# Optimization experiments

Hardware: AMD Instinct MI355X
Metric: run time of the kernel (lower is better)

## Reference

```python
import jax, jax.numpy as jnp
import numpy as np

N_NODES = 50000
N_EDGES = 800000
IN_DIM = 128
HID = 8
HEADS = 8
OUT_DIM = 64
NEG_SLOPE = 0.2


def setup_inputs() -> dict:
    key = jax.random.key(0)
    ks = jax.random.split(key, 8)
    x = jax.random.normal(ks[0], (N_NODES, IN_DIM), dtype=jnp.float32)
    edge_index = jax.random.randint(ks[1], (2, N_EDGES), 0, N_NODES, dtype=jnp.int64)
    W1 = jax.random.normal(ks[2], (IN_DIM, HEADS * HID), dtype=jnp.float32) / np.sqrt(IN_DIM)
    a_src1 = jax.random.normal(ks[3], (HEADS, HID), dtype=jnp.float32)
    a_dst1 = jax.random.normal(ks[4], (HEADS, HID), dtype=jnp.float32)
    b1 = jnp.zeros((HEADS * HID,), dtype=jnp.float32)
    W2 = jax.random.normal(ks[5], (HEADS * HID, OUT_DIM), dtype=jnp.float32) / np.sqrt(HEADS * HID)
    a_src2 = jax.random.normal(ks[6], (1, OUT_DIM), dtype=jnp.float32)
    a_dst2 = jax.random.normal(ks[7], (1, OUT_DIM), dtype=jnp.float32)
    b2 = jnp.zeros((OUT_DIM,), dtype=jnp.float32)
    return {"x": x, "edge_index": edge_index, "W1": W1, "a_src1": a_src1,
            "a_dst1": a_dst1, "b1": b1, "W2": W2, "a_src2": a_src2,
            "a_dst2": a_dst2, "b2": b2}


def gat_conv(x, src, dst, W, a_src, a_dst, b, heads, ch):
    # PyG GATConv (eval mode): linear -> per-edge LeakyReLU score ->
    # segment-softmax over incoming edges -> weighted scatter-add -> +bias
    n = x.shape[0]
    h = (x @ W).reshape(n, heads, ch)               # [N,H,C]
    score_src = jnp.einsum('nhc,hc->nh', h, a_src)  # [N,H]
    score_dst = jnp.einsum('nhc,hc->nh', h, a_dst)  # [N,H]
    e = jax.nn.leaky_relu(score_src[src] + score_dst[dst], NEG_SLOPE)  # [E,H]
    m = jax.ops.segment_max(e, dst, num_segments=n)
    m = jnp.where(jnp.isfinite(m), m, 0.0)
    p = jnp.exp(e - m[dst])
    denom = jax.ops.segment_sum(p, dst, num_segments=n)
    alpha = p / (denom[dst] + 1e-16)                # [E,H]
    out = jax.ops.segment_sum(h[src] * alpha[:, :, None], dst, num_segments=n)
    return out.reshape(n, heads * ch) + b


def reference(x, edge_index, W1, a_src1, a_dst1, b1, W2, a_src2, a_dst2, b2):
    n = x.shape[0]
    # add_self_loops=True (PyG default)
    loops = jnp.arange(n, dtype=edge_index.dtype)
    src = jnp.concatenate([edge_index[0], loops])
    dst = jnp.concatenate([edge_index[1], loops])
    h = gat_conv(x, src, dst, W1, a_src1, a_dst1, b1, HEADS, HID)
    h = jax.nn.elu(h)
    out = gat_conv(h, src, dst, W2, a_src2, a_dst2, b2, 1, OUT_DIM)
    return out
```

## Files before the change

### kernel.cpp

```cpp
#include <hip/hip_runtime.h>
#include <hip/hip_fp16.h>
#include <math.h>

#define N_NODES 50000
#define N_EDGES 800000
#define ET (N_EDGES + N_NODES)
#define IN_DIM 128
#define H1DIM 64
#define HEADS 8
#define HID 8
#define OUT_DIM 64
#define NEG_SLOPE 0.2f

#define SCAN_TILE 256
#define NTILES ((N_NODES + SCAN_TILE - 1) / SCAN_TILE)
#define RC 8
#define PF 6

#define LIN1_WAVES (N_NODES / 8)
#define LIN1_BLOCKS ((LIN1_WAVES + 3) / 4)
#define EB ((ET + 255) / 256)

__device__ __forceinline__ float lrelu(float v) { return v >= 0.f ? v : NEG_SLOPE * v; }

__device__ __forceinline__ float rdlane(float v, int l) {
    return __int_as_float(__builtin_amdgcn_readlane(__float_as_int(v), l));
}

__device__ __forceinline__ void fma8raw(uint4 u, float alpha, float* a) {
    float2 f0 = __half22float2(*(const __half2*)&u.x);
    float2 f1 = __half22float2(*(const __half2*)&u.y);
    float2 f2 = __half22float2(*(const __half2*)&u.z);
    float2 f3 = __half22float2(*(const __half2*)&u.w);
    a[0] += f0.x * alpha; a[1] += f0.y * alpha;
    a[2] += f1.x * alpha; a[3] += f1.y * alpha;
    a[4] += f2.x * alpha; a[5] += f2.y * alpha;
    a[6] += f3.x * alpha; a[7] += f3.y * alpha;
}

__device__ __forceinline__ void fma8h(const __half* __restrict__ base, float alpha, float* a) {
    fma8raw(*reinterpret_cast<const uint4*>(base), alpha, a);
}

__device__ __forceinline__ void edge_nodes(const int* __restrict__ ei, int e, int& s, int& d) {
    if (e < N_EDGES) { s = ei[e]; d = ei[N_EDGES + e]; }
    else             { s = e - N_EDGES; d = s; }
}


__global__ __launch_bounds__(256) void cl1_kernel(
    const int* __restrict__ ei, int* __restrict__ cnt, int* __restrict__ pos,
    const float* __restrict__ x, const float* __restrict__ W1,
    const float* __restrict__ a_src, const float* __restrict__ a_dst,
    __half* __restrict__ h1, float* __restrict__ ssrc, float* __restrict__ sdst)
{
    if (blockIdx.x >= LIN1_BLOCKS) {
        int i = (blockIdx.x - LIN1_BLOCKS) * 256 + threadIdx.x;
        if (i >= ET) return;
        int s, d; edge_nodes(ei, i, s, d);
        pos[i] = atomicAdd(&cnt[d], 1);
        return;
    }
    int wid = threadIdx.x >> 6, t = threadIdx.x & 63;
    int g = blockIdx.x * 4 + wid;
    if (g >= LIN1_WAVES) return;
    int n0 = g * 8;

    float x0[8], x1[8];
    #pragma unroll
    for (int nn = 0; nn < 8; ++nn) {
        x0[nn] = x[(n0 + nn) * IN_DIM + t];
        x1[nn] = x[(n0 + nn) * IN_DIM + 64 + t];
    }
    float acc[8] = {0,0,0,0,0,0,0,0};
    #pragma unroll 8
    for (int k = 0; k < 64; ++k) {
        float w = W1[k * 64 + t];
        #pragma unroll
        for (int nn = 0; nn < 8; ++nn) acc[nn] += rdlane(x0[nn], k) * w;
    }
    #pragma unroll 8
    for (int k = 0; k < 64; ++k) {
        float w = W1[(k + 64) * 64 + t];
        #pragma unroll
        for (int nn = 0; nn < 8; ++nn) acc[nn] += rdlane(x1[nn], k) * w;
    }

    float av = a_src[t], bv = a_dst[t];
    #pragma unroll
    for (int nn = 0; nn < 8; ++nn) {
        int n = n0 + nn;
        h1[n * 64 + t] = __float2half(acc[nn]);
        float rs = acc[nn] * av, rd = acc[nn] * bv;
        rs += __shfl_xor(rs, 1); rs += __shfl_xor(rs, 2); rs += __shfl_xor(rs, 4);
        rd += __shfl_xor(rd, 1); rd += __shfl_xor(rd, 2); rd += __shfl_xor(rd, 4);
        if ((t & 7) == 0) { ssrc[n * 8 + (t >> 3)] = rs; sdst[n * 8 + (t >> 3)] = rd; }
    }
}


__global__ __launch_bounds__(SCAN_TILE) void scanA_kernel(
    const int* __restrict__ cnt, int* __restrict__ row, int* __restrict__ aux)
{
    __shared__ int sh[SCAN_TILE];
    int t = threadIdx.x, i = blockIdx.x * SCAN_TILE + t;
    int v = (i < N_NODES) ? cnt[i] : 0;
    sh[t] = v;
    __syncthreads();
    #pragma unroll
    for (int off = 1; off < SCAN_TILE; off <<= 1) {
        int add = (t >= off) ? sh[t - off] : 0;
        __syncthreads();
        sh[t] += add;
        __syncthreads();
    }
    if (i < N_NODES) row[i] = sh[t] - v;
    if (t == SCAN_TILE - 1) aux[blockIdx.x] = sh[t];
}

__global__ __launch_bounds__(SCAN_TILE) void scanB_kernel(int* __restrict__ aux, int* __restrict__ row) {
    __shared__ int sh[SCAN_TILE];
    int t = threadIdx.x;
    int v = (t < NTILES) ? aux[t] : 0;
    sh[t] = v;
    __syncthreads();
    #pragma unroll
    for (int off = 1; off < SCAN_TILE; off <<= 1) {
        int add = (t >= off) ? sh[t - off] : 0;
        __syncthreads();
        sh[t] += add;
        __syncthreads();
    }
    if (t < NTILES) aux[t] = sh[t] - v;
    if (t == NTILES - 1) row[N_NODES] = sh[t];
}

__global__ __launch_bounds__(SCAN_TILE) void scanC_kernel(
    const int* __restrict__ aux, int* __restrict__ row)
{
    int i = blockIdx.x * SCAN_TILE + threadIdx.x;
    if (i >= N_NODES) return;
    row[i] += aux[i >> 8];
}

__global__ void fill_kernel(const int* __restrict__ ei, const int* __restrict__ row,
                            const int* __restrict__ pos, int* __restrict__ adj)
{
    int i = blockIdx.x * blockDim.x + threadIdx.x;
    if (i >= ET) return;
    int s, d; edge_nodes(ei, i, s, d);
    adj[row[d] + pos[i]] = s;
}


__global__ __launch_bounds__(256) void l1_kernel(
    const int* __restrict__ row, const int* __restrict__ adj,
    const __half* __restrict__ h1, const float* __restrict__ s1, const float* __restrict__ t1,
    const float* __restrict__ b1, const float* __restrict__ W2,
    const float* __restrict__ as2, const float* __restrict__ ad2,
    __half* __restrict__ h2, float* __restrict__ s2, float* __restrict__ t2)
{
    int wid = threadIdx.x >> 6, t = threadIdx.x & 63;
    int half = t >> 5, tt = t & 31;
    int n = blockIdx.x * 8 + wid * 2 + half;
    int beg = row[n], end = row[n + 1];
    int slot = tt >> 3, h = tt & 7;
    float sd = t1[n * 8 + h];
    const int e0 = beg + slot;
    const int hb = half << 5;

    int   sv[RC];
    float p[RC];
    uint4 raw[PF];
    float m = -3e38f;
    #pragma unroll
    for (int it = 0; it < RC; ++it) {
        int e = e0 + it * 4;
        bool ok = e < end;
        int s = ok ? adj[e] : n;
        sv[it] = s;
        float v = ok ? lrelu(s1[s * 8 + h] + sd) : -3e38f;
        p[it] = v;
        m = fmaxf(m, v);
        if (it < PF) raw[it] = *reinterpret_cast<const uint4*>(h1 + (size_t)s * 64 + h * 8);
    }
    for (int e = e0 + RC * 4; e < end; e += 4)
        m = fmaxf(m, lrelu(s1[adj[e] * 8 + h] + sd));
    m = fmaxf(m, __shfl_xor(m, 8));
    m = fmaxf(m, __shfl_xor(m, 16));

    float den = 0.f;
    #pragma unroll
    for (int it = 0; it < RC; ++it) {
        float pe = __expf(p[it] - m);
        p[it] = pe;
        den += pe;
    }
    for (int e = e0 + RC * 4; e < end; e += 4)
        den += __expf(lrelu(s1[adj[e] * 8 + h] + sd) - m);
    den += __shfl_xor(den, 8);
    den += __shfl_xor(den, 16);
    float inv = 1.f / (den + 1e-16f);

    float a[8] = {0,0,0,0,0,0,0,0};
    #pragma unroll
    for (int it = 0; it < PF; ++it) fma8raw(raw[it], p[it] * inv, a);
    #pragma unroll
    for (int it = PF; it < RC; ++it) {
        int e = e0 + it * 4;
        if (e < end) fma8h(h1 + (size_t)sv[it] * 64 + h * 8, p[it] * inv, a);
    }
    for (int e = e0 + RC * 4; e < end; e += 4) {
        int s = adj[e];
        float alpha = __expf(lrelu(s1[s * 8 + h] + sd) - m) * inv;
        fma8h(h1 + (size_t)s * 64 + h * 8, alpha, a);
    }
    #pragma unroll
    for (int j = 0; j < 8; ++j) {
        a[j] += __shfl_xor(a[j], 8);
        a[j] += __shfl_xor(a[j], 16);
    }

    float ha0 = 0.f, ha1 = 0.f;
    int srcA = hb + (tt >> 3);
    #pragma unroll
    for (int j = 0; j < 8; ++j) {
        float vA = __shfl(a[j], srcA);
        float vB = __shfl(a[j], srcA + 4);
        if ((tt & 7) == j) { ha0 = vA; ha1 = vB; }
    }

    ha0 += b1[tt];
    ha1 += b1[tt + 32];
    ha0 = ha0 > 0.f ? ha0 : (__expf(ha0) - 1.f);
    ha1 = ha1 > 0.f ? ha1 : (__expf(ha1) - 1.f);

    float c0 = 0.f, c1 = 0.f;
    #pragma unroll 8
    for (int k = 0; k < 32; ++k) {
        float w = __shfl(ha0, hb + k);
        c0 += w * W2[k * 64 + tt];
        c1 += w * W2[k * 64 + tt + 32];
    }
    #pragma unroll 8
    for (int k = 0; k < 32; ++k) {
        float w = __shfl(ha1, hb + k);
        c0 += w * W2[(k + 32) * 64 + tt];
        c1 += w * W2[(k + 32) * 64 + tt + 32];
    }
    h2[n * 64 + tt]      = __float2half(c0);
    h2[n * 64 + tt + 32] = __float2half(c1);

    float rs = c0 * as2[tt] + c1 * as2[tt + 32];
    float rd = c0 * ad2[tt] + c1 * ad2[tt + 32];
    #pragma unroll
    for (int mk = 16; mk >= 1; mk >>= 1) {
        rs += __shfl_xor(rs, mk);
        rd += __shfl_xor(rd, mk);
    }
    if (tt == 0) { s2[n] = rs; t2[n] = rd; }
}


__global__ __launch_bounds__(256) void l2_kernel(
    const int* __restrict__ row, const int* __restrict__ adj,
    const __half* __restrict__ h2, const float* __restrict__ s2, const float* __restrict__ t2,
    const float* __restrict__ b2, float* __restrict__ out)
{
    int wid = threadIdx.x >> 6, t = threadIdx.x & 63;
    int half = t >> 5, tt = t & 31;
    int n = blockIdx.x * 8 + wid * 2 + half;
    int beg = row[n], end = row[n + 1];
    int slot = tt >> 3, g = tt & 7;
    float sd = t2[n];
    const int e0 = beg + slot;

    int   sv[RC];
    float p[RC];
    uint4 raw[PF];
    float m = -3e38f;
    #pragma unroll
    for (int it = 0; it < RC; ++it) {
        int e = e0 + it * 4;
        bool ok = e < end;
        int s = ok ? adj[e] : n;
        sv[it] = s;
        float v = ok ? lrelu(s2[s] + sd) : -3e38f;
        p[it] = v;
        m = fmaxf(m, v);
        if (it < PF) raw[it] = *reinterpret_cast<const uint4*>(h2 + (size_t)s * 64 + g * 8);
    }
    for (int e = e0 + RC * 4; e < end; e += 4)
        m = fmaxf(m, lrelu(s2[adj[e]] + sd));
    m = fmaxf(m, __shfl_xor(m, 8));
    m = fmaxf(m, __shfl_xor(m, 16));

    float den = 0.f;
    #pragma unroll
    for (int it = 0; it < RC; ++it) {
        float pe = __expf(p[it] - m);
        p[it] = pe;
        den += pe;
    }
    for (int e = e0 + RC * 4; e < end; e += 4)
        den += __expf(lrelu(s2[adj[e]] + sd) - m);
    den += __shfl_xor(den, 8);
    den += __shfl_xor(den, 16);
    float inv = 1.f / (den + 1e-16f);

    float a[8] = {0,0,0,0,0,0,0,0};
    #pragma unroll
    for (int it = 0; it < PF; ++it) fma8raw(raw[it], p[it] * inv, a);
    #pragma unroll
    for (int it = PF; it < RC; ++it) {
        int e = e0 + it * 4;
        if (e < end) fma8h(h2 + (size_t)sv[it] * 64 + g * 8, p[it] * inv, a);
    }
    for (int e = e0 + RC * 4; e < end; e += 4) {
        int s = adj[e];
        float alpha = __expf(lrelu(s2[s] + sd) - m) * inv;
        fma8h(h2 + (size_t)s * 64 + g * 8, alpha, a);
    }
    #pragma unroll
    for (int j = 0; j < 8; ++j) {
        a[j] += __shfl_xor(a[j], 8);
        a[j] += __shfl_xor(a[j], 16);
    }
    if (slot == 0) {
        float4 o0 = make_float4(a[0] + b2[g * 8 + 0], a[1] + b2[g * 8 + 1],
                                a[2] + b2[g * 8 + 2], a[3] + b2[g * 8 + 3]);
        float4 o1 = make_float4(a[4] + b2[g * 8 + 4], a[5] + b2[g * 8 + 5],
                                a[6] + b2[g * 8 + 6], a[7] + b2[g * 8 + 7]);
        float4* op = (float4*)(out + (size_t)n * 64 + g * 8);
        op[0] = o0; op[1] = o1;
    }
}

extern "C" void kernel_launch(void* const* d_in, const int* in_sizes, int n_in,
                              void* d_out, int out_size, void* d_ws, size_t ws_size,
                              hipStream_t stream)
{
    const float* x   = (const float*)d_in[0];
    const int* ei    = (const int*)d_in[1];
    const float* W1  = (const float*)d_in[2];
    const float* as1 = (const float*)d_in[3];
    const float* ad1 = (const float*)d_in[4];
    const float* b1  = (const float*)d_in[5];
    const float* W2  = (const float*)d_in[6];
    const float* as2 = (const float*)d_in[7];
    const float* ad2 = (const float*)d_in[8];
    const float* b2  = (const float*)d_in[9];
    float* out = (float*)d_out;

    char* wsb = (char*)d_ws;
    __half* h1  = (__half*)wsb;
    __half* h2  = h1 + (size_t)N_NODES * 64;
    float*  s1  = (float*)(h2 + (size_t)N_NODES * 64);
    float*  t1  = s1 + N_NODES * 8;
    float*  s2  = t1 + N_NODES * 8;
    float*  t2  = s2 + N_NODES;
    int*    cnt = (int*)(t2 + N_NODES);
    int*    rowp = cnt + N_NODES;
    int*    aux  = rowp + N_NODES + 1;
    int*    adj  = aux + NTILES;
    int*    pos  = adj + ET;

    hipMemsetAsync(cnt, 0, N_NODES * sizeof(int), stream);

    cl1_kernel<<<LIN1_BLOCKS + EB, 256, 0, stream>>>(ei, cnt, pos, x, W1, as1, ad1, h1, s1, t1);

    scanA_kernel<<<NTILES, SCAN_TILE, 0, stream>>>(cnt, rowp, aux);
    scanB_kernel<<<1, SCAN_TILE, 0, stream>>>(aux, rowp);
    scanC_kernel<<<NTILES, SCAN_TILE, 0, stream>>>(aux, rowp);
    fill_kernel<<<EB, 256, 0, stream>>>(ei, rowp, pos, adj);

    l1_kernel<<<N_NODES / 8, 256, 0, stream>>>(rowp, adj, h1, s1, t1,
                                               b1, W2, as2, ad2, h2, s2, t2);

    l2_kernel<<<N_NODES / 8, 256, 0, stream>>>(rowp, adj, h2, s2, t2, b2, out);
}
```

Before: 231.0 us.

## Split degree counters into 8 replicas to spread atomic contention in CSR build

The degree-count atomics now go to one of 8 replicated counter arrays, chosen by block index, instead of a single array. The scan sums the 8 replicas, and scanC computes a per-replica starting offset so fill can place each edge without conflicts. Edge-count blocks are also moved ahead of the linear-layer blocks in the combined launch. This is meant to reduce atomic serialization on hot destination nodes, at the cost of a larger memset and 8x more counter reads and writes in the scans.

```diff
diff --git a/kernel.cpp b/kernel.cpp
--- a/kernel.cpp
+++ b/kernel.cpp
@@ -49,20 +49,20 @@
 
 
 __global__ __launch_bounds__(256) void cl1_kernel(
-    const int* __restrict__ ei, int* __restrict__ cnt, int* __restrict__ pos,
+    const int* __restrict__ ei, int* __restrict__ cnt8, int* __restrict__ pos,
     const float* __restrict__ x, const float* __restrict__ W1,
     const float* __restrict__ a_src, const float* __restrict__ a_dst,
     __half* __restrict__ h1, float* __restrict__ ssrc, float* __restrict__ sdst)
 {
-    if (blockIdx.x >= LIN1_BLOCKS) {
-        int i = (blockIdx.x - LIN1_BLOCKS) * 256 + threadIdx.x;
+    if (blockIdx.x < EB) {
+        int i = blockIdx.x * 256 + threadIdx.x;
         if (i >= ET) return;
         int s, d; edge_nodes(ei, i, s, d);
-        pos[i] = atomicAdd(&cnt[d], 1);
+        pos[i] = atomicAdd(&cnt8[(blockIdx.x & 7) * N_NODES + d], 1);
         return;
     }
     int wid = threadIdx.x >> 6, t = threadIdx.x & 63;
-    int g = blockIdx.x * 4 + wid;
+    int g = (blockIdx.x - EB) * 4 + wid;
     if (g >= LIN1_WAVES) return;
     int n0 = g * 8;
 
@@ -100,11 +100,15 @@
 
 
 __global__ __launch_bounds__(SCAN_TILE) void scanA_kernel(
-    const int* __restrict__ cnt, int* __restrict__ row, int* __restrict__ aux)
+    const int* __restrict__ cnt8, int* __restrict__ row, int* __restrict__ aux)
 {
     __shared__ int sh[SCAN_TILE];
     int t = threadIdx.x, i = blockIdx.x * SCAN_TILE + t;
-    int v = (i < N_NODES) ? cnt[i] : 0;
+    int v = 0;
+    if (i < N_NODES) {
+        #pragma unroll
+        for (int c = 0; c < 8; ++c) v += cnt8[c * N_NODES + i];
+    }
     sh[t] = v;
     __syncthreads();
     #pragma unroll
@@ -136,20 +140,29 @@
 }
 
 __global__ __launch_bounds__(SCAN_TILE) void scanC_kernel(
-    const int* __restrict__ aux, int* __restrict__ row)
+    const int* __restrict__ aux, int* __restrict__ row,
+    const int* __restrict__ cnt8, int* __restrict__ off8)
 {
     int i = blockIdx.x * SCAN_TILE + threadIdx.x;
     if (i >= N_NODES) return;
-    row[i] += aux[i >> 8];
-}
-
-__global__ void fill_kernel(const int* __restrict__ ei, const int* __restrict__ row,
+    int r = row[i] + aux[i >> 8];
+    row[i] = r;
+    int run = r;
+    #pragma unroll
+    for (int c = 0; c < 8; ++c) {
+        off8[c * N_NODES + i] = run;
+        run += cnt8[c * N_NODES + i];
+    }
+}
+
+__global__ void fill_kernel(const int* __restrict__ ei, const int* __restrict__ off8,
                             const int* __restrict__ pos, int* __restrict__ adj)
 {
     int i = blockIdx.x * blockDim.x + threadIdx.x;
     if (i >= ET) return;
     int s, d; edge_nodes(ei, i, s, d);
-    adj[row[d] + pos[i]] = s;
+    int c = (i >> 8) & 7;
+    adj[off8[c * N_NODES + d] + pos[i]] = s;
 }
 
 
@@ -359,20 +372,21 @@
     float*  t1  = s1 + N_NODES * 8;
     float*  s2  = t1 + N_NODES * 8;
     float*  t2  = s2 + N_NODES;
-    int*    cnt = (int*)(t2 + N_NODES);
-    int*    rowp = cnt + N_NODES;
+    int*    cnt8 = (int*)(t2 + N_NODES);
+    int*    off8 = cnt8 + 8 * N_NODES;
+    int*    rowp = off8 + 8 * N_NODES;
     int*    aux  = rowp + N_NODES + 1;
     int*    adj  = aux + NTILES;
     int*    pos  = adj + ET;
 
-    hipMemsetAsync(cnt, 0, N_NODES * sizeof(int), stream);
-
-    cl1_kernel<<<LIN1_BLOCKS + EB, 256, 0, stream>>>(ei, cnt, pos, x, W1, as1, ad1, h1, s1, t1);
-
-    scanA_kernel<<<NTILES, SCAN_TILE, 0, stream>>>(cnt, rowp, aux);
+    hipMemsetAsync(cnt8, 0, 8 * N_NODES * sizeof(int), stream);
+
+    cl1_kernel<<<EB + LIN1_BLOCKS, 256, 0, stream>>>(ei, cnt8, pos, x, W1, as1, ad1, h1, s1, t1);
+
+    scanA_kernel<<<NTILES, SCAN_TILE, 0, stream>>>(cnt8, rowp, aux);
     scanB_kernel<<<1, SCAN_TILE, 0, stream>>>(aux, rowp);
-    scanC_kernel<<<NTILES, SCAN_TILE, 0, stream>>>(aux, rowp);
-    fill_kernel<<<EB, 256, 0, stream>>>(ei, rowp, pos, adj);
+    scanC_kernel<<<NTILES, SCAN_TILE, 0, stream>>>(aux, rowp, cnt8, off8);
+    fill_kernel<<<EB, 256, 0, stream>>>(ei, off8, pos, adj);
 
     l1_kernel<<<N_NODES / 8, 256, 0, stream>>>(rowp, adj, h1, s1, t1,
                                                b1, W2, as2, ad2, h2, s2, t2);
```

After: 248.9 us. 7.7% more time.

## Assign 16 lanes per node in GAT aggregation kernels, four nodes per wave

Applied to the files above, without the earlier changes.

The layer-1 and layer-2 aggregation kernels now map each destination node to 16 lanes (two edge slots times eight head or feature groups) instead of 32. Each wave handles four nodes and the grid is halved. The register-cached edge window grows from 8 to 13 per slot. The early h-row prefetch (PF) is removed, so feature rows are loaded in the accumulation loop. The aim is to cut idle lanes, since average in-degree is about 17, and to halve the cross-lane reduction work. In exchange each lane walks more edges serially, which adds latency per node, and the W2 projection does twice the FMAs per lane.

```diff
diff --git a/kernel.cpp b/kernel.cpp
--- a/kernel.cpp
+++ b/kernel.cpp
@@ -6,16 +6,12 @@
 #define N_EDGES 800000
 #define ET (N_EDGES + N_NODES)
 #define IN_DIM 128
-#define H1DIM 64
 #define HEADS 8
-#define HID 8
-#define OUT_DIM 64
 #define NEG_SLOPE 0.2f
 
 #define SCAN_TILE 256
 #define NTILES ((N_NODES + SCAN_TILE - 1) / SCAN_TILE)
-#define RC 8
-#define PF 6
+#define RC 13
 
 #define LIN1_WAVES (N_NODES / 8)
 #define LIN1_BLOCKS ((LIN1_WAVES + 3) / 4)
@@ -27,7 +23,8 @@
     return __int_as_float(__builtin_amdgcn_readlane(__float_as_int(v), l));
 }
 
-__device__ __forceinline__ void fma8raw(uint4 u, float alpha, float* a) {
+__device__ __forceinline__ void fma8h(const __half* __restrict__ base, float alpha, float* a) {
+    uint4 u = *reinterpret_cast<const uint4*>(base);
     float2 f0 = __half22float2(*(const __half2*)&u.x);
     float2 f1 = __half22float2(*(const __half2*)&u.y);
     float2 f2 = __half22float2(*(const __half2*)&u.z);
@@ -38,10 +35,6 @@
     a[6] += f3.x * alpha; a[7] += f3.y * alpha;
 }
 
-__device__ __forceinline__ void fma8h(const __half* __restrict__ base, float alpha, float* a) {
-    fma8raw(*reinterpret_cast<const uint4*>(base), alpha, a);
-}
-
 __device__ __forceinline__ void edge_nodes(const int* __restrict__ ei, int e, int& s, int& d) {
     if (e < N_EDGES) { s = ei[e]; d = ei[N_EDGES + e]; }
     else             { s = e - N_EDGES; d = s; }
@@ -161,33 +154,30 @@
     __half* __restrict__ h2, float* __restrict__ s2, float* __restrict__ t2)
 {
     int wid = threadIdx.x >> 6, t = threadIdx.x & 63;
-    int half = t >> 5, tt = t & 31;
-    int n = blockIdx.x * 8 + wid * 2 + half;
+    int q = t >> 4, tt = t & 15;
+    int n = blockIdx.x * 16 + wid * 4 + q;
     int beg = row[n], end = row[n + 1];
     int slot = tt >> 3, h = tt & 7;
     float sd = t1[n * 8 + h];
     const int e0 = beg + slot;
-    const int hb = half << 5;
+    const int qb = q << 4;
 
     int   sv[RC];
     float p[RC];
-    uint4 raw[PF];
     float m = -3e38f;
     #pragma unroll
     for (int it = 0; it < RC; ++it) {
-        int e = e0 + it * 4;
+        int e = e0 + it * 2;
         bool ok = e < end;
         int s = ok ? adj[e] : n;
         sv[it] = s;
         float v = ok ? lrelu(s1[s * 8 + h] + sd) : -3e38f;
         p[it] = v;
         m = fmaxf(m, v);
-        if (it < PF) raw[it] = *reinterpret_cast<const uint4*>(h1 + (size_t)s * 64 + h * 8);
-    }
-    for (int e = e0 + RC * 4; e < end; e += 4)
+    }
+    for (int e = e0 + RC * 2; e < end; e += 2)
         m = fmaxf(m, lrelu(s1[adj[e] * 8 + h] + sd));
     m = fmaxf(m, __shfl_xor(m, 8));
-    m = fmaxf(m, __shfl_xor(m, 16));
 
     float den = 0.f;
     #pragma unroll
@@ -196,65 +186,66 @@
         p[it] = pe;
         den += pe;
     }
-    for (int e = e0 + RC * 4; e < end; e += 4)
+    for (int e = e0 + RC * 2; e < end; e += 2)
         den += __expf(lrelu(s1[adj[e] * 8 + h] + sd) - m);
     den += __shfl_xor(den, 8);
-    den += __shfl_xor(den, 16);
     float inv = 1.f / (den + 1e-16f);
 
     float a[8] = {0,0,0,0,0,0,0,0};
     #pragma unroll
-    for (int it = 0; it < PF; ++it) fma8raw(raw[it], p[it] * inv, a);
-    #pragma unroll
-    for (int it = PF; it < RC; ++it) {
-        int e = e0 + it * 4;
+    for (int it = 0; it < RC; ++it) {
+        int e = e0 + it * 2;
         if (e < end) fma8h(h1 + (size_t)sv[it] * 64 + h * 8, p[it] * inv, a);
     }
-    for (int e = e0 + RC * 4; e < end; e += 4) {
+    for (int e = e0 + RC * 2; e < end; e += 2) {
         int s = adj[e];
         float alpha = __expf(lrelu(s1[s * 8 + h] + sd) - m) * inv;
         fma8h(h1 + (size_t)s * 64 + h * 8, alpha, a);
     }
     #pragma unroll
+    for (int j = 0; j < 8; ++j) a[j] += __shfl_xor(a[j], 8);
+
+    float ha[4] = {0,0,0,0};
+    int src0 = qb + (tt >> 3);
+    #pragma unroll
     for (int j = 0; j < 8; ++j) {
-        a[j] += __shfl_xor(a[j], 8);
-        a[j] += __shfl_xor(a[j], 16);
-    }
-
-    float ha0 = 0.f, ha1 = 0.f;
-    int srcA = hb + (tt >> 3);
-    #pragma unroll
-    for (int j = 0; j < 8; ++j) {
-        float vA = __shfl(a[j], srcA);
-        float vB = __shfl(a[j], srcA + 4);
-        if ((tt & 7) == j) { ha0 = vA; ha1 = vB; }
-    }
-
-    ha0 += b1[tt];
-    ha1 += b1[tt + 32];
-    ha0 = ha0 > 0.f ? ha0 : (__expf(ha0) - 1.f);
-    ha1 = ha1 > 0.f ? ha1 : (__expf(ha1) - 1.f);
-
-    float c0 = 0.f, c1 = 0.f;
-    #pragma unroll 8
-    for (int k = 0; k < 32; ++k) {
-        float w = __shfl(ha0, hb + k);
-        c0 += w * W2[k * 64 + tt];
-        c1 += w * W2[k * 64 + tt + 32];
-    }
-    #pragma unroll 8
-    for (int k = 0; k < 32; ++k) {
-        float w = __shfl(ha1, hb + k);
-        c0 += w * W2[(k + 32) * 64 + tt];
-        c1 += w * W2[(k + 32) * 64 + tt + 32];
-    }
-    h2[n * 64 + tt]      = __float2half(c0);
-    h2[n * 64 + tt + 32] = __float2half(c1);
-
-    float rs = c0 * as2[tt] + c1 * as2[tt + 32];
-    float rd = c0 * ad2[tt] + c1 * ad2[tt + 32];
-    #pragma unroll
-    for (int mk = 16; mk >= 1; mk >>= 1) {
+        float v0 = __shfl(a[j], src0);
+        float v1 = __shfl(a[j], src0 + 2);
+        float v2 = __shfl(a[j], src0 + 4);
+        float v3 = __shfl(a[j], src0 + 6);
+        if ((tt & 7) == j) { ha[0] = v0; ha[1] = v1; ha[2] = v2; ha[3] = v3; }
+    }
+
+    #pragma unroll
+    for (int c = 0; c < 4; ++c) {
+        float v = ha[c] + b1[tt + 16 * c];
+        ha[c] = v > 0.f ? v : (__expf(v) - 1.f);
+    }
+
+    float c2[4] = {0,0,0,0};
+    #pragma unroll
+    for (int cr = 0; cr < 4; ++cr) {
+        #pragma unroll 8
+        for (int kk = 0; kk < 16; ++kk) {
+            float w = __shfl(ha[cr], qb + kk);
+            int k = cr * 16 + kk;
+            c2[0] += w * W2[k * 64 + tt];
+            c2[1] += w * W2[k * 64 + tt + 16];
+            c2[2] += w * W2[k * 64 + tt + 32];
+            c2[3] += w * W2[k * 64 + tt + 48];
+        }
+    }
+    #pragma unroll
+    for (int c = 0; c < 4; ++c) h2[n * 64 + tt + 16 * c] = __float2half(c2[c]);
+
+    float rs = 0.f, rd = 0.f;
+    #pragma unroll
+    for (int c = 0; c < 4; ++c) {
+        rs += c2[c] * as2[tt + 16 * c];
+        rd += c2[c] * ad2[tt + 16 * c];
+    }
+    #pragma unroll
+    for (int mk = 8; mk >= 1; mk >>= 1) {
         rs += __shfl_xor(rs, mk);
         rd += __shfl_xor(rd, mk);
     }
@@ -268,8 +259,8 @@
     const float* __restrict__ b2, float* __restrict__ out)
 {
     int wid = threadIdx.x >> 6, t = threadIdx.x & 63;
-    int half = t >> 5, tt = t & 31;
-    int n = blockIdx.x * 8 + wid * 2 + half;
+    int q = t >> 4, tt = t & 15;
+    int n = blockIdx.x * 16 + wid * 4 + q;
     int beg = row[n], end = row[n + 1];
     int slot = tt >> 3, g = tt & 7;
     float sd = t2[n];
@@ -277,23 +268,20 @@
 
     int   sv[RC];
     float p[RC];
-    uint4 raw[PF];
     float m = -3e38f;
     #pragma unroll
     for (int it = 0; it < RC; ++it) {
-        int e = e0 + it * 4;
+        int e = e0 + it * 2;
         bool ok = e < end;
         int s = ok ? adj[e] : n;
         sv[it] = s;
         float v = ok ? lrelu(s2[s] + sd) : -3e38f;
         p[it] = v;
         m = fmaxf(m, v);
-        if (it < PF) raw[it] = *reinterpret_cast<const uint4*>(h2 + (size_t)s * 64 + g * 8);
-    }
-    for (int e = e0 + RC * 4; e < end; e += 4)
+    }
+    for (int e = e0 + RC * 2; e < end; e += 2)
         m = fmaxf(m, lrelu(s2[adj[e]] + sd));
     m = fmaxf(m, __shfl_xor(m, 8));
-    m = fmaxf(m, __shfl_xor(m, 16));
 
     float den = 0.f;
     #pragma unroll
@@ -302,30 +290,25 @@
         p[it] = pe;
         den += pe;
     }
-    for (int e = e0 + RC * 4; e < end; e += 4)
+    for (int e = e0 + RC * 2; e < end; e += 2)
         den += __expf(lrelu(s2[adj[e]] + sd) - m);
     den += __shfl_xor(den, 8);
-    den += __shfl_xor(den, 16);
     float inv = 1.f / (den + 1e-16f);
 
     float a[8] = {0,0,0,0,0,0,0,0};
     #pragma unroll
-    for (int it = 0; it < PF; ++it) fma8raw(raw[it], p[it] * inv, a);
-    #pragma unroll
-    for (int it = PF; it < RC; ++it) {
-        int e = e0 + it * 4;
+    for (int it = 0; it < RC; ++it) {
+        int e = e0 + it * 2;
         if (e < end) fma8h(h2 + (size_t)sv[it] * 64 + g * 8, p[it] * inv, a);
     }
-    for (int e = e0 + RC * 4; e < end; e += 4) {
+    for (int e = e0 + RC * 2; e < end; e += 2) {
         int s = adj[e];
         float alpha = __expf(lrelu(s2[s] + sd) - m) * inv;
         fma8h(h2 + (size_t)s * 64 + g * 8, alpha, a);
     }
     #pragma unroll
-    for (int j = 0; j < 8; ++j) {
-        a[j] += __shfl_xor(a[j], 8);
-        a[j] += __shfl_xor(a[j], 16);
-    }
+    for (int j = 0; j < 8; ++j) a[j] += __shfl_xor(a[j], 8);
+
     if (slot == 0) {
         float4 o0 = make_float4(a[0] + b2[g * 8 + 0], a[1] + b2[g * 8 + 1],
                                 a[2] + b2[g * 8 + 2], a[3] + b2[g * 8 + 3]);
@@ -374,8 +357,8 @@
     scanC_kernel<<<NTILES, SCAN_TILE, 0, stream>>>(aux, rowp);
     fill_kernel<<<EB, 256, 0, stream>>>(ei, rowp, pos, adj);
 
-    l1_kernel<<<N_NODES / 8, 256, 0, stream>>>(rowp, adj, h1, s1, t1,
-                                               b1, W2, as2, ad2, h2, s2, t2);
-
-    l2_kernel<<<N_NODES / 8, 256, 0, stream>>>(rowp, adj, h2, s2, t2, b2, out);
-}
+    l1_kernel<<<N_NODES / 16, 256, 0, stream>>>(rowp, adj, h1, s1, t1,
+                                                b1, W2, as2, ad2, h2, s2, t2);
+
+    l2_kernel<<<N_NODES / 16, 256, 0, stream>>>(rowp, adj, h2, s2, t2, b2, out);
+}
```

Measured after the change: 238.1 us. 1.03x slower.
